# Performance work log

Measured on AMD Instinct MI355X. Metric: run time of the kernel, lower is better.

Reference implementation:

```python
import jax, jax.numpy as jnp
import numpy as np

LAT_T, LAT_H, LAT_W = 16, 44, 80  # hard-coded latent grid in preprocess_mask


def _preprocess_mask(mask):
    """mask: [T, H, W, B] float video mask -> [B, S] binary mask, S = 16*44*80.
    Mirrors torch trilinear interpolate (align_corners=False) per temporal chunk."""
    m = jnp.transpose(mask, (3, 0, 1, 2))[:, None]  # [B,1,T,H,W]
    B, _, T, _, _ = m.shape
    tgt = (B, 1, 1, LAT_H, LAT_W)
    pieces = [jax.image.resize(m[:, :, :1], tgt, 'trilinear', antialias=False)]
    for wi in range(1, T, 8):
        pieces.append(jax.image.resize(m[:, :, wi:wi + 8], tgt, 'trilinear', antialias=False))
    mm = jnp.concatenate(pieces, axis=2)[:, 0]  # [B,16,44,80]
    return (mm > 0.5).astype(jnp.float32).reshape(B, -1)  # [B,S]


def setup_inputs() -> dict:
    key = jax.random.key(0)
    ks = jax.random.split(key, 6)
    B, S, H, D, P, R = 1, 56320, 8, 64, 128, 2
    T, MH, MW = 121, 88, 160
    return {
        'q': jax.random.normal(ks[0], (B, S, H, D), jnp.float32),
        'k': jax.random.normal(ks[1], (B, P, H, D), jnp.float32),
        'v': jax.random.normal(ks[2], (B, P, H, D), jnp.float32),
        'regional_k': jax.random.normal(ks[3], (R, B, P, H, D), jnp.float32),
        'regional_v': jax.random.normal(ks[4], (R, B, P, H, D), jnp.float32),
        'region_masks': jax.random.uniform(ks[5], (R, T, MH, MW, B), jnp.float32),
    }


def reference(q, k, v, regional_k, regional_v, region_masks):
    B, S, H, D = q.shape
    P = k.shape[1]
    R = regional_k.shape[0]
    scale = D ** -0.5
    base_ratio = 0.5

    # per-region binary masks over the latent sequence: [R,B,S]
    masks = jnp.stack([_preprocess_mask(region_masks[i]) for i in range(R)], axis=0)
    masks_b = masks > 0.5
    global_mask = masks.sum(axis=0) == 0  # [B,S] queries covered by no region
    # allowed[b,s,r]: segment r of combined KV (r=0 global prompt, r>=1 region r-1)
    allowed = jnp.concatenate([global_mask[..., None], jnp.moveaxis(masks_b, 0, -1)], axis=-1)  # [B,S,R+1]

    combined_k = jnp.concatenate([k[None], regional_k], axis=0)  # [R+1,B,P,H,D]
    combined_v = jnp.concatenate([v[None], regional_v], axis=0)

    # regional pass: scores [B,H,S,R+1,P], additive -inf bias per segment
    scores = jnp.einsum('bshd,rbphd->bhsrp', q, combined_k) * scale
    scores = jnp.where(allowed[:, None, :, :, None], scores, -jnp.inf)
    p = jax.nn.softmax(scores.reshape(B, H, S, (R + 1) * P), axis=-1)
    out_reg = jnp.einsum('bhsrp,rbphd->bshd', p.reshape(B, H, S, R + 1, P), combined_v)

    # base pass: plain cross attention over the global prompt
    s_base = jnp.einsum('bshd,bphd->bhsp', q, k) * scale
    out_base = jnp.einsum('bhsp,bphd->bshd', jax.nn.softmax(s_base, axis=-1), v)

    out = out_reg * (1.0 - base_ratio) + out_base * base_ratio
    return out.reshape(B, S, H * D)
```

## Files before the change

kernel.cpp:

```cpp
#include <hip/hip_runtime.h>

typedef short short8  __attribute__((ext_vector_type(8)));
typedef short short4v __attribute__((ext_vector_type(4)));
typedef float f32x4   __attribute__((ext_vector_type(4)));

#define MFMA_BF16(A,B,C) __builtin_amdgcn_mfma_f32_16x16x32_bf16((A),(B),(C),0,0,0)

__device__ __forceinline__ short bf16bits(float f){
  return (short)__builtin_bit_cast(unsigned short, static_cast<__bf16>(f));
}

#define EXP_SCORE(s, BIAS) __builtin_amdgcn_exp2f(__builtin_fmaf((s), 0.18033688011112042f, (BIAS)))
#define EXP_C2 (-11.541560327111707f)

__global__ __launch_bounds__(256) void prep_kernel(const float* __restrict__ rm,
                                                   const float* __restrict__ k,
                                                   const float* __restrict__ v,
                                                   const float* __restrict__ rk,
                                                   const float* __restrict__ rv,
                                                   unsigned* __restrict__ allowed,
                                                   unsigned short* __restrict__ Kb,
                                                   unsigned short* __restrict__ VT){
  const int bid = blockIdx.x;
  if (bid < 220){
    int s = bid*256 + threadIdx.x;
    if (s >= 56320) return;
    int t = s / 3520;
    int rem = s - t*3520;
    int i = rem / 80;
    int j = rem - i*80;
    int y = 2*i, x = 2*j;
    bool bin[2];
    #pragma unroll
    for (int r=0;r<2;r++){
      const float* base = rm + (size_t)r*121*88*160;
      float acc;
      if (t == 0){
        const float* p0 = base + (size_t)(0*88 + y)*160 + x;
        acc = 0.25f*(p0[0]+p0[1]+p0[160]+p0[161]);
      } else {
        const float* pa = base + (size_t)((8*t-4)*88 + y)*160 + x;
        const float* pb = base + (size_t)((8*t-3)*88 + y)*160 + x;
        acc = 0.125f*(pa[0]+pa[1]+pa[160]+pa[161] + pb[0]+pb[1]+pb[160]+pb[161]);
      }
      bin[r] = acc > 0.5f;
    }
    unsigned bits = (bin[0]||bin[1]) ? 0u : 1u;
    if (bin[0]) bits |= 2u;
    if (bin[1]) bits |= 4u;
    allowed[s] = bits;
  } else {
    int idx = (bid-220)*256 + threadIdx.x;
    if (idx >= 3*128*8*64) return;
    int d   = idx & 63;
    int h   = (idx >> 6) & 7;
    int p   = (idx >> 9) & 127;
    int seg = idx >> 16;
    int low = idx & 65535;
    float kv_, vv_;
    if (seg == 0){ kv_ = k[low];                          vv_ = v[low]; }
    else         { kv_ = rk[(size_t)(seg-1)*65536 + low]; vv_ = rv[(size_t)(seg-1)*65536 + low]; }
    const int kk = seg*128 + p;
    Kb[(size_t)h*24576 + ((kk>>4)*2 + (d>>5))*512
       + ((((d>>3)&3)*16) + (kk&15))*8 + (d&7)] = (unsigned short)bf16bits(kv_);
    {
      const int kkc = kk & 31;
      const int Qv  = (kkc >> 2) & 3;
      const int jv  = (kkc & 3) | ((kkc & 16) >> 2);
      VT[(size_t)h*24576 + ((kk>>5)*4 + (d>>4))*512
         + (Qv*16 + (d&15))*8 + jv] = (unsigned short)bf16bits(vv_);
    }
  }
}

__global__ __launch_bounds__(512)
void attn_kernel(const float* __restrict__ q,
                 const unsigned* __restrict__ allowed,
                 const unsigned short* __restrict__ Kb,
                 const unsigned short* __restrict__ VT,
                 float* __restrict__ out){
  const int h    = blockIdx.y;
  const int wave = threadIdx.x >> 6;
  const int lane = threadIdx.x & 63;
  const int c    = lane & 15;
  const int Q    = lane >> 4;

  __shared__ __align__(16) char Ks[49152];

  const int s = blockIdx.x*128 + wave*16 + c;

  const char* kg = (const char*)Kb + (size_t)h*49152;
  short8 st0 = *(const short8*)(kg + wave*6144 + 0*1024 + lane*16);
  short8 st1 = *(const short8*)(kg + wave*6144 + 1*1024 + lane*16);
  short8 st2 = *(const short8*)(kg + wave*6144 + 2*1024 + lane*16);
  short8 st3 = *(const short8*)(kg + wave*6144 + 3*1024 + lane*16);
  short8 st4 = *(const short8*)(kg + wave*6144 + 4*1024 + lane*16);
  short8 st5 = *(const short8*)(kg + wave*6144 + 5*1024 + lane*16);

  const unsigned ab = allowed[s];
  const float* qp = q + ((size_t)s*8 + h)*64 + Q*8;
  f32x4 q0 = *(const f32x4*)(qp);
  f32x4 q1 = *(const f32x4*)(qp+4);
  f32x4 q2 = *(const f32x4*)(qp+32);
  f32x4 q3 = *(const f32x4*)(qp+36);
  short8 f0, f1;
  #pragma unroll
  for (int j=0;j<4;j++){
    f0[j] = bf16bits(q0[j]); f0[4+j] = bf16bits(q1[j]);
    f1[j] = bf16bits(q2[j]); f1[4+j] = bf16bits(q3[j]);
  }

  *(short8*)(Ks + wave*6144 + 0*1024 + lane*16) = st0;
  *(short8*)(Ks + wave*6144 + 1*1024 + lane*16) = st1;
  *(short8*)(Ks + wave*6144 + 2*1024 + lane*16) = st2;
  *(short8*)(Ks + wave*6144 + 3*1024 + lane*16) = st3;
  *(short8*)(Ks + wave*6144 + 4*1024 + lane*16) = st4;
  *(short8*)(Ks + wave*6144 + 5*1024 + lane*16) = st5;

  const char* kfb = Ks + lane*16;
  const char* vgf = (const char*)VT + (size_t)h*49152 + lane*16;

  short8 v0, v1, v2, v3;
#define VLOAD(kc)                                                     \
  v0 = *(const short8*)(vgf + ((kc)*4+0)*1024);                       \
  v1 = *(const short8*)(vgf + ((kc)*4+1)*1024);                       \
  v2 = *(const short8*)(vgf + ((kc)*4+2)*1024);                       \
  v3 = *(const short8*)(vgf + ((kc)*4+3)*1024);                       \
      \
  __builtin_amdgcn_sched_barrier(0x38F);

#define CHUNK(kc, LSUM, BIAS, ACC)                                    \
  {                                                                   \
    short8 kf0 = *(const short8*)(kfb + ((kc)*4+0)*1024);             \
    short8 kf1 = *(const short8*)(kfb + ((kc)*4+1)*1024);             \
    short8 kf2 = *(const short8*)(kfb + ((kc)*4+2)*1024);             \
    short8 kf3 = *(const short8*)(kfb + ((kc)*4+3)*1024);             \
    f32x4 sA = {0,0,0,0}; sA = MFMA_BF16(kf0,f0,sA); sA = MFMA_BF16(kf1,f1,sA); \
    f32x4 sB = {0,0,0,0}; sB = MFMA_BF16(kf2,f0,sB); sB = MFMA_BF16(kf3,f1,sB); \
    short8 pf;                                                        \
    _Pragma("unroll")                                                 \
    for (int r=0;r<4;r++){                                            \
      float eA = EXP_SCORE(sA[r], BIAS); LSUM += eA; pf[r]   = bf16bits(eA); \
      float eB = EXP_SCORE(sB[r], BIAS); LSUM += eB; pf[4+r] = bf16bits(eB); \
    }                                                                 \
    ACC[0] = MFMA_BF16(v0, pf, ACC[0]);                               \
    ACC[1] = MFMA_BF16(v1, pf, ACC[1]);                               \
    ACC[2] = MFMA_BF16(v2, pf, ACC[2]);                               \
    ACC[3] = MFMA_BF16(v3, pf, ACC[3]);                               \
  }

  VLOAD(0);

  __syncthreads();

  const float bias1 = ((ab>>1)&1u) ? EXP_C2 : -3.0e38f;
  const float bias2 = ((ab>>2)&1u) ? EXP_C2 : -3.0e38f;

  float lb=0.f, lr=0.f;
  f32x4 a0[4], a1[4];
  #pragma unroll
  for (int m=0;m<4;m++){ a0[m]=(f32x4){0,0,0,0}; a1[m]=(f32x4){0,0,0,0}; }

  CHUNK(0,  lb, EXP_C2, a0); VLOAD(1);
  CHUNK(1,  lb, EXP_C2, a0); VLOAD(2);
  CHUNK(2,  lb, EXP_C2, a0); VLOAD(3);
  CHUNK(3,  lb, EXP_C2, a0); VLOAD(4);
  CHUNK(4,  lr, bias1,  a1); VLOAD(5);
  CHUNK(5,  lr, bias1,  a1); VLOAD(6);
  CHUNK(6,  lr, bias1,  a1); VLOAD(7);
  CHUNK(7,  lr, bias1,  a1); VLOAD(8);
  CHUNK(8,  lr, bias2,  a1); VLOAD(9);
  CHUNK(9,  lr, bias2,  a1); VLOAD(10);
  CHUNK(10, lr, bias2,  a1); VLOAD(11);
  CHUNK(11, lr, bias2,  a1);

  lb += __shfl_xor(lb,16); lb += __shfl_xor(lb,32);
  lr += __shfl_xor(lr,16); lr += __shfl_xor(lr,32);

  const float invb = 0.5f/lb;
  const float lreg = ((ab&1u)? lb : 0.f) + lr;
  const float invr = 0.5f/lreg;
  const float cA   = invb + ((ab&1u)? invr : 0.f);

  float* ob = out + (size_t)s*512 + h*64 + Q*4;
  #pragma unroll
  for (int m=0;m<4;m++){
    f32x4 o;
    #pragma unroll
    for (int r=0;r<4;r++) o[r] = a0[m][r]*cA + a1[m][r]*invr;
    *(f32x4*)(ob + m*16) = o;
  }
}

extern "C" void kernel_launch(void* const* d_in, const int* in_sizes, int n_in,
                              void* d_out, int out_size, void* d_ws, size_t ws_size,
                              hipStream_t stream) {
  const float* q  = (const float*)d_in[0];
  const float* k  = (const float*)d_in[1];
  const float* v  = (const float*)d_in[2];
  const float* rk = (const float*)d_in[3];
  const float* rv = (const float*)d_in[4];
  const float* rm = (const float*)d_in[5];
  float* out = (float*)d_out;

  char* ws = (char*)d_ws;
  unsigned*       allowed = (unsigned*)ws;
  unsigned short* Kb      = (unsigned short*)(ws + 225280);
  unsigned short* VT      = (unsigned short*)(ws + 225280 + 393216);

  prep_kernel<<<988, 256, 0, stream>>>(rm, k, v, rk, rv, allowed, Kb, VT);
  dim3 grid(440, 8);
  attn_kernel<<<grid, 512, 0, stream>>>(q, allowed, Kb, VT, out);
}
```

Measured before the change: 260.9 us.

## Switch attention to 32x32x16 MFMA with LDS-staged base accumulator and direct global-to-LDS K load

Replaces the 16x16x32 bf16 MFMA tiles with 32x32x16 tiles, so each wave handles 32 queries and a block uses 4 waves (256 threads) instead of 8. K and V are re-laid-out in the prep kernel to match the new fragment layout. K is copied straight into LDS with global_load_lds rather than through registers. The base-segment accumulator is spilled to a new 32 KB LDS buffer so the regional accumulator can reuse the same registers. The larger MFMA shape cuts instruction count, but LDS use per block rises to 80 KB, which may limit occupancy.

```diff
diff --git a/kernel.cpp b/kernel.cpp
--- a/kernel.cpp
+++ b/kernel.cpp
@@ -1,10 +1,10 @@
 #include <hip/hip_runtime.h>
 
 typedef short short8  __attribute__((ext_vector_type(8)));
-typedef short short4v __attribute__((ext_vector_type(4)));
 typedef float f32x4   __attribute__((ext_vector_type(4)));
-
-#define MFMA_BF16(A,B,C) __builtin_amdgcn_mfma_f32_16x16x32_bf16((A),(B),(C),0,0,0)
+typedef float f32x16  __attribute__((ext_vector_type(16)));
+
+#define MFMA32(A,B,C) __builtin_amdgcn_mfma_f32_32x32x16_bf16((A),(B),(C),0,0,0)
 
 __device__ __forceinline__ short bf16bits(float f){
   return (short)__builtin_bit_cast(unsigned short, static_cast<__bf16>(f));
@@ -61,19 +61,24 @@
     if (seg == 0){ kv_ = k[low];                          vv_ = v[low]; }
     else         { kv_ = rk[(size_t)(seg-1)*65536 + low]; vv_ = rv[(size_t)(seg-1)*65536 + low]; }
     const int kk = seg*128 + p;
-    Kb[(size_t)h*24576 + ((kk>>4)*2 + (d>>5))*512
-       + ((((d>>3)&3)*16) + (kk&15))*8 + (d&7)] = (unsigned short)bf16bits(kv_);
     {
-      const int kkc = kk & 31;
-      const int Qv  = (kkc >> 2) & 3;
-      const int jv  = (kkc & 3) | ((kkc & 16) >> 2);
-      VT[(size_t)h*24576 + ((kk>>5)*4 + (d>>4))*512
-         + (Qv*16 + (d&15))*8 + jv] = (unsigned short)bf16bits(vv_);
-    }
-  }
-}
-
-__global__ __launch_bounds__(512)
+      const int f  = d >> 4, hi = (d >> 3) & 1, j = d & 7;
+      Kb[(size_t)h*24576 + ((kk>>5)*4 + f)*512
+         + (hi*32 + (kk&31))*8 + j] = (unsigned short)bf16bits(kv_);
+    }
+    {
+      const int kap = kk & 31;
+      const int kh  = kap >> 4, rem = kap & 15;
+      const int hi  = (rem >> 2) & 1;
+      const int e   = (rem & 3) + 4*(rem >> 3);
+      const int dblk = d >> 5;
+      VT[(size_t)h*24576 + ((kk>>5)*4 + dblk*2 + kh)*512
+         + (hi*32 + (d&31))*8 + e] = (unsigned short)bf16bits(vv_);
+    }
+  }
+}
+
+__global__ __launch_bounds__(256)
 void attn_kernel(const float* __restrict__ q,
                  const unsigned* __restrict__ allowed,
                  const unsigned short* __restrict__ Kb,
@@ -82,43 +87,48 @@
   const int h    = blockIdx.y;
   const int wave = threadIdx.x >> 6;
   const int lane = threadIdx.x & 63;
-  const int c    = lane & 15;
-  const int Q    = lane >> 4;
+  const int qc   = lane & 31;
+  const int hi   = lane >> 5;
 
   __shared__ __align__(16) char Ks[49152];
-
-  const int s = blockIdx.x*128 + wave*16 + c;
-
-  const char* kg = (const char*)Kb + (size_t)h*49152;
-  short8 st0 = *(const short8*)(kg + wave*6144 + 0*1024 + lane*16);
-  short8 st1 = *(const short8*)(kg + wave*6144 + 1*1024 + lane*16);
-  short8 st2 = *(const short8*)(kg + wave*6144 + 2*1024 + lane*16);
-  short8 st3 = *(const short8*)(kg + wave*6144 + 3*1024 + lane*16);
-  short8 st4 = *(const short8*)(kg + wave*6144 + 4*1024 + lane*16);
-  short8 st5 = *(const short8*)(kg + wave*6144 + 5*1024 + lane*16);
+  __shared__ __align__(16) char A0s[32768];
+
+  const int s = blockIdx.x*128 + wave*32 + qc;
+
+  {
+    typedef __attribute__((address_space(1))) const unsigned int gu32_t;
+    typedef __attribute__((address_space(3))) unsigned int lu32_t;
+    const char* kg = (const char*)Kb + (size_t)h*49152;
+    #pragma unroll
+    for (int i=0;i<12;i++){
+      const int ub = wave*12288 + i*1024;
+      __builtin_amdgcn_global_load_lds((gu32_t*)(kg + ub + lane*16),
+                                       (lu32_t*)(Ks + ub), 16, 0, 0);
+    }
+  }
 
   const unsigned ab = allowed[s];
-  const float* qp = q + ((size_t)s*8 + h)*64 + Q*8;
-  f32x4 q0 = *(const f32x4*)(qp);
-  f32x4 q1 = *(const f32x4*)(qp+4);
-  f32x4 q2 = *(const f32x4*)(qp+32);
-  f32x4 q3 = *(const f32x4*)(qp+36);
-  short8 f0, f1;
-  #pragma unroll
-  for (int j=0;j<4;j++){
-    f0[j] = bf16bits(q0[j]); f0[4+j] = bf16bits(q1[j]);
-    f1[j] = bf16bits(q2[j]); f1[4+j] = bf16bits(q3[j]);
-  }
-
-  *(short8*)(Ks + wave*6144 + 0*1024 + lane*16) = st0;
-  *(short8*)(Ks + wave*6144 + 1*1024 + lane*16) = st1;
-  *(short8*)(Ks + wave*6144 + 2*1024 + lane*16) = st2;
-  *(short8*)(Ks + wave*6144 + 3*1024 + lane*16) = st3;
-  *(short8*)(Ks + wave*6144 + 4*1024 + lane*16) = st4;
-  *(short8*)(Ks + wave*6144 + 5*1024 + lane*16) = st5;
+  const float* qp = q + ((size_t)s*8 + h)*64 + hi*8;
+  short8 qf0, qf1, qf2, qf3;
+  {
+    f32x4 a, b;
+    a = *(const f32x4*)(qp);      b = *(const f32x4*)(qp+4);
+    #pragma unroll
+    for (int j=0;j<4;j++){ qf0[j]=bf16bits(a[j]); qf0[4+j]=bf16bits(b[j]); }
+    a = *(const f32x4*)(qp+16);   b = *(const f32x4*)(qp+20);
+    #pragma unroll
+    for (int j=0;j<4;j++){ qf1[j]=bf16bits(a[j]); qf1[4+j]=bf16bits(b[j]); }
+    a = *(const f32x4*)(qp+32);   b = *(const f32x4*)(qp+36);
+    #pragma unroll
+    for (int j=0;j<4;j++){ qf2[j]=bf16bits(a[j]); qf2[4+j]=bf16bits(b[j]); }
+    a = *(const f32x4*)(qp+48);   b = *(const f32x4*)(qp+52);
+    #pragma unroll
+    for (int j=0;j<4;j++){ qf3[j]=bf16bits(a[j]); qf3[4+j]=bf16bits(b[j]); }
+  }
 
   const char* kfb = Ks + lane*16;
   const char* vgf = (const char*)VT + (size_t)h*49152 + lane*16;
+  char*       pk  = A0s + wave*8192 + lane*16;
 
   short8 v0, v1, v2, v3;
 #define VLOAD(kc)                                                     \
@@ -126,27 +136,29 @@
   v1 = *(const short8*)(vgf + ((kc)*4+1)*1024);                       \
   v2 = *(const short8*)(vgf + ((kc)*4+2)*1024);                       \
   v3 = *(const short8*)(vgf + ((kc)*4+3)*1024);                       \
-      \
   __builtin_amdgcn_sched_barrier(0x38F);
 
-#define CHUNK(kc, LSUM, BIAS, ACC)                                    \
+#define CHUNK(kc, LSUM, BIAS)                                         \
   {                                                                   \
     short8 kf0 = *(const short8*)(kfb + ((kc)*4+0)*1024);             \
     short8 kf1 = *(const short8*)(kfb + ((kc)*4+1)*1024);             \
     short8 kf2 = *(const short8*)(kfb + ((kc)*4+2)*1024);             \
     short8 kf3 = *(const short8*)(kfb + ((kc)*4+3)*1024);             \
-    f32x4 sA = {0,0,0,0}; sA = MFMA_BF16(kf0,f0,sA); sA = MFMA_BF16(kf1,f1,sA); \
-    f32x4 sB = {0,0,0,0}; sB = MFMA_BF16(kf2,f0,sB); sB = MFMA_BF16(kf3,f1,sB); \
-    short8 pf;                                                        \
+    f32x16 sa = {0,0,0,0,0,0,0,0,0,0,0,0,0,0,0,0};                    \
+    sa = MFMA32(kf0, qf0, sa);                                        \
+    sa = MFMA32(kf1, qf1, sa);                                        \
+    sa = MFMA32(kf2, qf2, sa);                                        \
+    sa = MFMA32(kf3, qf3, sa);                                        \
+    short8 pf0, pf1;                                                  \
     _Pragma("unroll")                                                 \
-    for (int r=0;r<4;r++){                                            \
-      float eA = EXP_SCORE(sA[r], BIAS); LSUM += eA; pf[r]   = bf16bits(eA); \
-      float eB = EXP_SCORE(sB[r], BIAS); LSUM += eB; pf[4+r] = bf16bits(eB); \
+    for (int r=0;r<8;r++){                                            \
+      float e0 = EXP_SCORE(sa[r],   BIAS); LSUM += e0; pf0[r] = bf16bits(e0); \
+      float e1 = EXP_SCORE(sa[8+r], BIAS); LSUM += e1; pf1[r] = bf16bits(e1); \
     }                                                                 \
-    ACC[0] = MFMA_BF16(v0, pf, ACC[0]);                               \
-    ACC[1] = MFMA_BF16(v1, pf, ACC[1]);                               \
-    ACC[2] = MFMA_BF16(v2, pf, ACC[2]);                               \
-    ACC[3] = MFMA_BF16(v3, pf, ACC[3]);                               \
+    acc0 = MFMA32(v0, pf0, acc0);                                     \
+    acc0 = MFMA32(v1, pf1, acc0);                                     \
+    acc1 = MFMA32(v2, pf0, acc1);                                     \
+    acc1 = MFMA32(v3, pf1, acc1);                                     \
   }
 
   VLOAD(0);
@@ -156,39 +168,55 @@
   const float bias1 = ((ab>>1)&1u) ? EXP_C2 : -3.0e38f;
   const float bias2 = ((ab>>2)&1u) ? EXP_C2 : -3.0e38f;
 
-  float lb=0.f, lr=0.f;
-  f32x4 a0[4], a1[4];
+  float lb = 0.f, lr = 0.f;
+  f32x16 acc0 = {0,0,0,0,0,0,0,0,0,0,0,0,0,0,0,0};
+  f32x16 acc1 = {0,0,0,0,0,0,0,0,0,0,0,0,0,0,0,0};
+
+  CHUNK(0, lb, EXP_C2); VLOAD(1);
+  CHUNK(1, lb, EXP_C2); VLOAD(2);
+  CHUNK(2, lb, EXP_C2); VLOAD(3);
+  CHUNK(3, lb, EXP_C2); VLOAD(4);
+
   #pragma unroll
-  for (int m=0;m<4;m++){ a0[m]=(f32x4){0,0,0,0}; a1[m]=(f32x4){0,0,0,0}; }
-
-  CHUNK(0,  lb, EXP_C2, a0); VLOAD(1);
-  CHUNK(1,  lb, EXP_C2, a0); VLOAD(2);
-  CHUNK(2,  lb, EXP_C2, a0); VLOAD(3);
-  CHUNK(3,  lb, EXP_C2, a0); VLOAD(4);
-  CHUNK(4,  lr, bias1,  a1); VLOAD(5);
-  CHUNK(5,  lr, bias1,  a1); VLOAD(6);
-  CHUNK(6,  lr, bias1,  a1); VLOAD(7);
-  CHUNK(7,  lr, bias1,  a1); VLOAD(8);
-  CHUNK(8,  lr, bias2,  a1); VLOAD(9);
-  CHUNK(9,  lr, bias2,  a1); VLOAD(10);
-  CHUNK(10, lr, bias2,  a1); VLOAD(11);
-  CHUNK(11, lr, bias2,  a1);
-
-  lb += __shfl_xor(lb,16); lb += __shfl_xor(lb,32);
-  lr += __shfl_xor(lr,16); lr += __shfl_xor(lr,32);
+  for (int g=0; g<4; ++g){
+    f32x4 t0 = {acc0[g*4+0], acc0[g*4+1], acc0[g*4+2], acc0[g*4+3]};
+    f32x4 t1 = {acc1[g*4+0], acc1[g*4+1], acc1[g*4+2], acc1[g*4+3]};
+    *(f32x4*)(pk + (g  )*1024) = t0;
+    *(f32x4*)(pk + (g+4)*1024) = t1;
+  }
+  acc0 = (f32x16){0,0,0,0,0,0,0,0,0,0,0,0,0,0,0,0};
+  acc1 = (f32x16){0,0,0,0,0,0,0,0,0,0,0,0,0,0,0,0};
+
+  CHUNK(4,  lr, bias1); VLOAD(5);
+  CHUNK(5,  lr, bias1); VLOAD(6);
+  CHUNK(6,  lr, bias1); VLOAD(7);
+  CHUNK(7,  lr, bias1); VLOAD(8);
+  CHUNK(8,  lr, bias2); VLOAD(9);
+  CHUNK(9,  lr, bias2); VLOAD(10);
+  CHUNK(10, lr, bias2); VLOAD(11);
+  CHUNK(11, lr, bias2);
+
+  lb += __shfl_xor(lb, 32);
+  lr += __shfl_xor(lr, 32);
 
   const float invb = 0.5f/lb;
   const float lreg = ((ab&1u)? lb : 0.f) + lr;
   const float invr = 0.5f/lreg;
   const float cA   = invb + ((ab&1u)? invr : 0.f);
 
-  float* ob = out + (size_t)s*512 + h*64 + Q*4;
+  float* ob = out + (size_t)s*512 + h*64 + hi*4;
   #pragma unroll
-  for (int m=0;m<4;m++){
-    f32x4 o;
-    #pragma unroll
-    for (int r=0;r<4;r++) o[r] = a0[m][r]*cA + a1[m][r]*invr;
-    *(f32x4*)(ob + m*16) = o;
+  for (int g=0; g<4; ++g){
+    f32x4 a0v = *(const f32x4*)(pk + (g  )*1024);
+    f32x4 a1v = *(const f32x4*)(pk + (g+4)*1024);
+    f32x4 o0, o1;
+    #pragma unroll
+    for (int r=0;r<4;r++){
+      o0[r] = a0v[r]*cA + acc0[g*4+r]*invr;
+      o1[r] = a1v[r]*cA + acc1[g*4+r]*invr;
+    }
+    *(f32x4*)(ob + g*8)      = o0;
+    *(f32x4*)(ob + 32 + g*8) = o1;
   }
 }
 
@@ -210,5 +238,5 @@
 
   prep_kernel<<<988, 256, 0, stream>>>(rm, k, v, rk, rv, allowed, Kb, VT);
   dim3 grid(440, 8);
-  attn_kernel<<<grid, 512, 0, stream>>>(q, allowed, Kb, VT, out);
-}
+  attn_kernel<<<grid, 256, 0, stream>>>(q, allowed, Kb, VT, out);
+}
```

Result: no change. 263.4 us (+0.9%).
